# Performance work log

Measured on AMD Instinct MI355X. Metric: run time of the kernel, lower is better.

## Reference

```python
import jax, jax.numpy as jnp
import numpy as np

BETA = 0.25

def setup_inputs() -> dict:
    key = jax.random.key(0)
    k1, k2 = jax.random.split(key)
    x = jax.random.normal(k1, (32, 1024, 256), dtype=jnp.float32)
    # tf.random_uniform_initializer default range is [-0.05, 0.05)
    embedding = jax.random.uniform(k2, (256, 8192), dtype=jnp.float32, minval=-0.05, maxval=0.05)
    return {"x": x, "embedding": embedding}


def reference(x, embedding):
    # x: [B, S, D]; embedding: [D, K] (codebook stored column-wise, as in the tf module)
    D = x.shape[-1]
    flat = x.reshape(-1, D)                                   # [N, D]
    dists = (jnp.sum(flat * flat, axis=1, keepdims=True)
             - 2.0 * (flat @ embedding)
             + jnp.sum(embedding * embedding, axis=0))
    idx = jnp.argmin(dists, axis=1)                           # [N] int
    quantized = jnp.take(embedding.T, idx, axis=0).reshape(x.shape)  # gather codebook columns
    # VQ losses
    commitment = jnp.mean(jnp.square(jax.lax.stop_gradient(quantized) - x))
    codebook = jnp.mean(jnp.square(quantized - jax.lax.stop_gradient(x)))
    loss = BETA * commitment + codebook
    # straight-through estimator
    quantized_st = x + jax.lax.stop_gradient(quantized - x)
    return quantized_st, loss
```

## Files before the change

kernel.cpp:

```cpp
#include <hip/hip_runtime.h>

typedef float f4   __attribute__((ext_vector_type(4)));
typedef float f2   __attribute__((ext_vector_type(2)));
typedef _Float16 f16x8 __attribute__((ext_vector_type(8)));
typedef float f32x4  __attribute__((ext_vector_type(4)));

#define N_ROWS  32768
#define D_DIM   256
#define K_CODES 8192
#define NUM_ELEM (N_ROWS * D_DIM)
#define EPS_MARGIN 2e-3f
#define FB_CAP  8192
#define FB_RPB  16
#define RF_SLICES 32
#define N_PANELS 256
#define HALF_PANELS 128

__device__ __forceinline__ void gl2lds16(const void* g, void* l) {
    __builtin_amdgcn_global_load_lds(
        (const __attribute__((address_space(1))) unsigned int*)g,
        (__attribute__((address_space(3))) unsigned int*)l, 16, 0, 0);
}

__global__ void prep_kernel(const float* __restrict__ E, short* __restrict__ Ep,
                            float* __restrict__ Et32, float* __restrict__ ee,
                            float* __restrict__ ctl) {
    __shared__ float eepart[8][32];
    const int p  = blockIdx.x;
    const int t  = threadIdx.x;
    const int c  = t & 31;
    const int gq = t >> 5;
    const int cp = p * 32;
    if (p == 0) {
        f4 z = (f4)(0.0f);
        f4* dst = (f4*)ctl;
        dst[t * 2]     = z;
        dst[t * 2 + 1] = z;
    }
    short* ph = Ep + (size_t)p * 8192;
    float ss = 0.0f;
    #pragma unroll
    for (int gi = 0; gi < 4; ++gi) {
        int g = gq * 4 + gi;
        f16x8 h;
        f4 av, bv;
        #pragma unroll
        for (int j = 0; j < 8; ++j) {
            float v = E[(size_t)(g * 8 + j) * K_CODES + cp + c];
            h[j] = (_Float16)v;
            ss += v * v;
            if (j < 4) av[j] = v; else bv[j - 4] = v;
        }
        *(f16x8*)(ph + (g * 32 + c) * 8) = h;
        *(f4*)(Et32 + (size_t)(cp + c) * D_DIM + g * 8)     = av;
        *(f4*)(Et32 + (size_t)(cp + c) * D_DIM + g * 8 + 4) = bv;
    }
    eepart[gq][c] = ss;
    __syncthreads();
    if (t < 32) {
        float s = 0.0f;
        #pragma unroll
        for (int q = 0; q < 8; ++q) s += eepart[q][t];
        ee[cp + t] = s;
    }
}

__launch_bounds__(256, 2)
__global__ void mfma_sieve_kernel(const float* __restrict__ X,
                                  const short* __restrict__ Ep,
                                  const float* __restrict__ ee,
                                  f2* __restrict__ res_bs,
                                  int* __restrict__ res_idx) {
    __shared__ __align__(16) short Bbuf[2][8192];
    const int t    = threadIdx.x;
    const int w    = t >> 6;
    const int lane = t & 63;
    const int n    = lane & 15;
    const int quad = lane >> 4;
    const int half = blockIdx.x & 1;
    const int row0 = (blockIdx.x >> 1) * 128;
    const int rw   = row0 + w * 32;
    const int p0   = half * HALF_PANELS;

    f16x8 Ah[2][8];
    #pragma unroll
    for (int rt = 0; rt < 2; ++rt) {
        const float* xp = X + (size_t)(rw + rt * 16 + n) * D_DIM;
        #pragma unroll
        for (int ks = 0; ks < 8; ++ks) {
            int d = ks * 32 + quad * 8;
            f4 a = *(const f4*)(xp + d);
            f4 b = *(const f4*)(xp + d + 4);
            f16x8 h;
            #pragma unroll
            for (int j = 0; j < 8; ++j) {
                float x = (j < 4) ? a[j] : b[j - 4];
                h[j] = (_Float16)x;
            }
            Ah[rt][ks] = h;
        }
    }

    float bestv[8], secv[8]; int besti[8];
    #pragma unroll
    for (int s = 0; s < 8; ++s) { bestv[s] = 1e30f; secv[s] = 1e30f; besti[s] = 0; }

    {
        const char* gp = (const char*)Ep + (size_t)p0 * 16384;
        char* lp = (char*)&Bbuf[0][0];
        #pragma unroll
        for (int i = 0; i < 4; ++i)
            gl2lds16(gp + (w * 4 + i) * 1024 + lane * 16, lp + (w * 4 + i) * 1024);
    }
    __syncthreads();

    for (int i = 0; i < HALF_PANELS; ++i) {
        const int p   = p0 + i;
        const int buf = i & 1;
        if (i + 1 < HALF_PANELS) {
            const char* gp = (const char*)Ep + (size_t)(p + 1) * 16384;
            char* lp = (char*)&Bbuf[buf ^ 1][0];
            #pragma unroll
            for (int k = 0; k < 4; ++k)
                gl2lds16(gp + (w * 4 + k) * 1024 + lane * 16, lp + (w * 4 + k) * 1024);
        }

        const short* Bh = &Bbuf[buf][0];

        f32x4 acc[2][2];
        #pragma unroll
        for (int ct = 0; ct < 2; ++ct)
            #pragma unroll
            for (int rt = 0; rt < 2; ++rt)
                acc[ct][rt] = (f32x4)(0.0f);

        #pragma unroll
        for (int ks = 0; ks < 8; ++ks) {
            const int g = ks * 4 + quad;
            f16x8 bh[2];
            #pragma unroll
            for (int ct = 0; ct < 2; ++ct) {
                int c = ct * 16 + n;
                bh[ct] = *(const f16x8*)(Bh + (g * 32 + c) * 8);
            }
            #pragma unroll
            for (int ct = 0; ct < 2; ++ct)
                #pragma unroll
                for (int rt = 0; rt < 2; ++rt)
                    acc[ct][rt] = __builtin_amdgcn_mfma_f32_16x16x32_f16(Ah[rt][ks], bh[ct], acc[ct][rt], 0, 0, 0);
        }

        const int cb = p * 32;
        #pragma unroll
        for (int ct = 0; ct < 2; ++ct) {
            int code = cb + ct * 16 + n;
            float eev = ee[code];
            #pragma unroll
            for (int rt = 0; rt < 2; ++rt)
                #pragma unroll
                for (int r = 0; r < 4; ++r) {
                    float key = fmaf(-2.0f, acc[ct][rt][r], eev);
                    int s = rt * 4 + r;
                    float nb = fminf(key, bestv[s]);
                    secv[s]  = fminf(secv[s], fmaxf(key, bestv[s]));
                    besti[s] = (key < bestv[s]) ? code : besti[s];
                    bestv[s] = nb;
                }
        }
        __syncthreads();
    }

    #pragma unroll
    for (int off = 1; off < 16; off <<= 1) {
        #pragma unroll
        for (int s = 0; s < 8; ++s) {
            float ov = __shfl_xor(bestv[s], off);
            int   oi = __shfl_xor(besti[s], off);
            float os = __shfl_xor(secv[s], off);
            bool owin = (ov < bestv[s]) || (ov == bestv[s] && oi < besti[s]);
            if (owin) { secv[s] = fminf(os, bestv[s]); bestv[s] = ov; besti[s] = oi; }
            else      { secv[s] = fminf(secv[s], ov); }
        }
    }

    if (n == 0) {
        #pragma unroll
        for (int s = 0; s < 8; ++s) {
            int rl  = w * 32 + (s >> 2) * 16 + quad * 4 + (s & 3);
            int row = row0 + rl;
            f2 bs; bs[0] = bestv[s]; bs[1] = secv[s];
            res_bs[(size_t)row * 2 + half]  = bs;
            res_idx[(size_t)row * 2 + half] = besti[s];
        }
    }
}

__global__ void gather_kernel(const float* __restrict__ X, const float* __restrict__ Et32,
                              const f2* __restrict__ res_bs, const int* __restrict__ res_idx,
                              int* __restrict__ counter, int2* __restrict__ list,
                              float* __restrict__ out, double* __restrict__ loss_sum) {
    __shared__ int bl_[128];
    const int t    = threadIdx.x;
    const int row0 = blockIdx.x * 128;
    if (t < 128) {
        const int row = row0 + t;
        f2 a = res_bs[(size_t)row * 2];
        f2 b = res_bs[(size_t)row * 2 + 1];
        int ia = res_idx[(size_t)row * 2];
        int ib = res_idx[(size_t)row * 2 + 1];
        float gb; int gi; float gs;
        if (b[0] < a[0]) { gb = b[0]; gi = ib; gs = fminf(b[1], a[0]); }
        else             { gb = a[0]; gi = ia; gs = fminf(a[1], b[0]); }
        bl_[t] = gi;
        if (gs - gb <= EPS_MARGIN) {
            int pos = atomicAdd(counter, 1);
            if (pos < FB_CAP) list[pos] = make_int2(row, gi);
        }
    }
    __syncthreads();
    double ls = 0.0;
    const int d = t;
    #pragma unroll 4
    for (int r = 0; r < 128; ++r) {
        int code = bl_[r];
        float q  = Et32[(size_t)code * D_DIM + d];
        float x  = X[(size_t)(row0 + r) * D_DIM + d];
        float dq = q - x;
        out[(size_t)(row0 + r) * D_DIM + d] = x + dq;
        ls += (double)dq * (double)dq;
    }
    #pragma unroll
    for (int off = 32; off > 0; off >>= 1)
        ls += __shfl_down(ls, off);
    if ((t & 63) == 0) atomicAdd(loss_sum, ls);
}

__global__ void refine1_kernel(const float* __restrict__ X, const float* __restrict__ E,
                               const int* __restrict__ counter, const int2* __restrict__ list,
                               double* __restrict__ res_v, int* __restrict__ res_i) {
    __shared__ double xt[FB_RPB][D_DIM];
    __shared__ int rows_sh[FB_RPB];
    __shared__ double wbv[4][FB_RPB];
    __shared__ int    wbi[4][FB_RPB];

    int nf = *counter; if (nf > FB_CAP) nf = FB_CAP;
    const int nchunks = (nf + FB_RPB - 1) / FB_RPB;
    const int nitems  = nchunks * RF_SLICES;
    const int t = threadIdx.x;

    for (int item = blockIdx.x; item < nitems; item += gridDim.x) {
        const int rc = item / RF_SLICES;
        const int sl = item % RF_SLICES;
        __syncthreads();
        if (t < FB_RPB) {
            int e = rc * FB_RPB + t;
            int2 ent = list[(e < nf) ? e : 0];
            rows_sh[t] = ent.x;
        }
        __syncthreads();
        #pragma unroll
        for (int j = 0; j < FB_RPB; ++j)
            xt[j][t] = (double)X[(size_t)rows_sh[j] * D_DIM + t];
        __syncthreads();

        const int k0 = sl * 256 + t;
        double s[FB_RPB], q = 0.0;
        #pragma unroll
        for (int j = 0; j < FB_RPB; ++j) s[j] = 0.0;
        for (int d = 0; d < D_DIM; ++d) {
            double e0d = (double)E[(size_t)d * K_CODES + k0];
            q += e0d * e0d;
            #pragma unroll
            for (int j = 0; j < FB_RPB; ++j)
                s[j] += xt[j][d] * e0d;
        }
        double bv[FB_RPB]; int bi[FB_RPB];
        #pragma unroll
        for (int j = 0; j < FB_RPB; ++j) { bv[j] = q - 2.0 * s[j]; bi[j] = k0; }
        #pragma unroll
        for (int off = 1; off < 64; off <<= 1) {
            #pragma unroll
            for (int j = 0; j < FB_RPB; ++j) {
                double ov = __shfl_xor(bv[j], off);
                int    oi = __shfl_xor(bi[j], off);
                if (ov < bv[j] || (ov == bv[j] && oi < bi[j])) { bv[j] = ov; bi[j] = oi; }
            }
        }
        const int wave = t >> 6;
        if ((t & 63) == 0) {
            #pragma unroll
            for (int j = 0; j < FB_RPB; ++j) { wbv[wave][j] = bv[j]; wbi[wave][j] = bi[j]; }
        }
        __syncthreads();
        if (t < FB_RPB) {
            double b = wbv[0][t]; int i_ = wbi[0][t];
            #pragma unroll
            for (int wv = 1; wv < 4; ++wv) {
                double ov = wbv[wv][t]; int oi = wbi[wv][t];
                if (ov < b || (ov == b && oi < i_)) { b = ov; i_ = oi; }
            }
            int e = rc * FB_RPB + t;
            res_v[(size_t)e * RF_SLICES + sl] = b;
            res_i[(size_t)e * RF_SLICES + sl] = i_;
        }
    }
}

__global__ void patch_kernel(const float* __restrict__ X, const float* __restrict__ Et32,
                             float* __restrict__ out, double* __restrict__ loss_sum,
                             const int* __restrict__ counter, const int2* __restrict__ list,
                             const double* __restrict__ res_v, const int* __restrict__ res_i) {
    int nf = *counter; if (nf > FB_CAP) nf = FB_CAP;
    __shared__ int nc_sh;
    const int t = threadIdx.x;
    for (int b = blockIdx.x; b < nf; b += gridDim.x) {
        __syncthreads();
        if (t == 0) {
            double bv = res_v[(size_t)b * RF_SLICES]; int bi = res_i[(size_t)b * RF_SLICES];
            for (int s = 1; s < RF_SLICES; ++s) {
                double v = res_v[(size_t)b * RF_SLICES + s];
                int    i = res_i[(size_t)b * RF_SLICES + s];
                if (v < bv || (v == bv && i < bi)) { bv = v; bi = i; }
            }
            nc_sh = bi;
        }
        __syncthreads();
        int2 ent = list[b];
        const int oc = ent.y, row = ent.x, nc = nc_sh;
        if (nc != oc) {
            float x  = X[(size_t)row * D_DIM + t];
            float qn = Et32[(size_t)nc * D_DIM + t];
            float qo = Et32[(size_t)oc * D_DIM + t];
            float dqn = qn - x, dqo = qo - x;
            out[(size_t)row * D_DIM + t] = x + dqn;
            double dl = (double)dqn * dqn - (double)dqo * dqo;
            #pragma unroll
            for (int off = 32; off > 0; off >>= 1)
                dl += __shfl_down(dl, off);
            if ((t & 63) == 0) atomicAdd(loss_sum, dl);
        }
    }
}

__global__ void fin_kernel(const double* __restrict__ loss_sum, float* __restrict__ out) {
    double m = loss_sum[0] / (double)NUM_ELEM;
    out[NUM_ELEM] = (float)(0.25 * m + m);
}

extern "C" void kernel_launch(void* const* d_in, const int* in_sizes, int n_in,
                              void* d_out, int out_size, void* d_ws, size_t ws_size,
                              hipStream_t stream) {
    const float* X = (const float*)d_in[0];
    const float* E = (const float*)d_in[1];
    float* out = (float*)d_out;

    double* loss_sum = (double*)d_ws;
    int*    counter  = (int*)((char*)d_ws + 8);
    float*  ee       = (float*)((char*)d_ws + 8192);
    int2*   list     = (int2*)((char*)d_ws + 40960);
    double* res_v    = (double*)((char*)d_ws + 131072);
    int*    res_i    = (int*)((char*)d_ws + 2228224);
    float*  Et32     = (float*)((char*)d_ws + 4194304);
    short*  Ep       = (short*)((char*)d_ws + 12582912);
    f2*     res_bs   = (f2*)((char*)d_ws + 16777216);
    int*    res_idx  = (int*)((char*)d_ws + 17301504);

    prep_kernel<<<N_PANELS, 256, 0, stream>>>(E, Ep, Et32, ee, (float*)d_ws);
    mfma_sieve_kernel<<<512, 256, 0, stream>>>(X, Ep, ee, res_bs, res_idx);
    gather_kernel<<<N_ROWS / 128, 256, 0, stream>>>(X, Et32, res_bs, res_idx,
                                                    counter, list, out, loss_sum);
    refine1_kernel<<<1024, 256, 0, stream>>>(X, E, counter, list, res_v, res_i);
    patch_kernel<<<1024, 256, 0, stream>>>(X, Et32, out, loss_sum, counter, list,
                                           res_v, res_i);
    fin_kernel<<<1, 1, 0, stream>>>(loss_sum, out);
}
```

Measured before the change: 329.5 us.

## Fuse gather into sieve via last-arriver counter and fold finalize into patch

The separate gather kernel is removed. Each 128-row tile's two half-codebook sieve blocks bump a per-tile ready counter, and the second block to arrive merges both halves and writes the output rows and loss. The finalize kernel is likewise folded into the patch kernel, where the last block to finish computes the loss. This removes two kernel launches and lets gather work overlap with sieve blocks still running. In exchange it adds atomics and fences, and relies on the ready and patch_done counters being zeroed in workspace every call.

New measurement: 503.7 us. 52.9% more time.

```diff
diff --git a/kernel.cpp b/kernel.cpp
--- a/kernel.cpp
+++ b/kernel.cpp
@@ -69,16 +69,23 @@
 __global__ void mfma_sieve_kernel(const float* __restrict__ X,
                                   const short* __restrict__ Ep,
                                   const float* __restrict__ ee,
+                                  const float* __restrict__ Et32,
                                   f2* __restrict__ res_bs,
-                                  int* __restrict__ res_idx) {
+                                  int* __restrict__ res_idx,
+                                  int* __restrict__ ready,
+                                  int* __restrict__ counter, int2* __restrict__ list,
+                                  float* __restrict__ out, double* __restrict__ loss_sum) {
     __shared__ __align__(16) short Bbuf[2][8192];
+    __shared__ int bl2_[128];
+    __shared__ int do_gather;
     const int t    = threadIdx.x;
     const int w    = t >> 6;
     const int lane = t & 63;
     const int n    = lane & 15;
     const int quad = lane >> 4;
     const int half = blockIdx.x & 1;
-    const int row0 = (blockIdx.x >> 1) * 128;
+    const int rtile = blockIdx.x >> 1;
+    const int row0 = rtile * 128;
     const int rw   = row0 + w * 32;
     const int p0   = half * HALF_PANELS;
 
@@ -193,25 +200,29 @@
             res_idx[(size_t)row * 2 + half] = besti[s];
         }
     }
-}
-
-__global__ void gather_kernel(const float* __restrict__ X, const float* __restrict__ Et32,
-                              const f2* __restrict__ res_bs, const int* __restrict__ res_idx,
-                              int* __restrict__ counter, int2* __restrict__ list,
-                              float* __restrict__ out, double* __restrict__ loss_sum) {
-    __shared__ int bl_[128];
-    const int t    = threadIdx.x;
-    const int row0 = blockIdx.x * 128;
+
+    __threadfence();
+    __syncthreads();
+    if (t == 0) {
+        int old = atomicAdd(&ready[rtile], 1);
+        do_gather = (old == 1);
+    }
+    __syncthreads();
+    if (!do_gather) return;
+    __threadfence();
+
     if (t < 128) {
         const int row = row0 + t;
-        f2 a = res_bs[(size_t)row * 2];
-        f2 b = res_bs[(size_t)row * 2 + 1];
-        int ia = res_idx[(size_t)row * 2];
-        int ib = res_idx[(size_t)row * 2 + 1];
+        union { double d; f2 f; } ua, ub;
+        ua.d = atomicAdd((double*)&res_bs[(size_t)row * 2], 0.0);
+        ub.d = atomicAdd((double*)&res_bs[(size_t)row * 2 + 1], 0.0);
+        int ia = atomicOr(&res_idx[(size_t)row * 2], 0);
+        int ib = atomicOr(&res_idx[(size_t)row * 2 + 1], 0);
+        f2 a = ua.f, b = ub.f;
         float gb; int gi; float gs;
         if (b[0] < a[0]) { gb = b[0]; gi = ib; gs = fminf(b[1], a[0]); }
         else             { gb = a[0]; gi = ia; gs = fminf(a[1], b[0]); }
-        bl_[t] = gi;
+        bl2_[t] = gi;
         if (gs - gb <= EPS_MARGIN) {
             int pos = atomicAdd(counter, 1);
             if (pos < FB_CAP) list[pos] = make_int2(row, gi);
@@ -222,7 +233,7 @@
     const int d = t;
     #pragma unroll 4
     for (int r = 0; r < 128; ++r) {
-        int code = bl_[r];
+        int code = bl2_[r];
         float q  = Et32[(size_t)code * D_DIM + d];
         float x  = X[(size_t)(row0 + r) * D_DIM + d];
         float dq = q - x;
@@ -309,7 +320,8 @@
 __global__ void patch_kernel(const float* __restrict__ X, const float* __restrict__ Et32,
                              float* __restrict__ out, double* __restrict__ loss_sum,
                              const int* __restrict__ counter, const int2* __restrict__ list,
-                             const double* __restrict__ res_v, const int* __restrict__ res_i) {
+                             const double* __restrict__ res_v, const int* __restrict__ res_i,
+                             int* __restrict__ patch_done) {
     int nf = *counter; if (nf > FB_CAP) nf = FB_CAP;
     __shared__ int nc_sh;
     const int t = threadIdx.x;
@@ -340,11 +352,15 @@
             if ((t & 63) == 0) atomicAdd(loss_sum, dl);
         }
     }
-}
-
-__global__ void fin_kernel(const double* __restrict__ loss_sum, float* __restrict__ out) {
-    double m = loss_sum[0] / (double)NUM_ELEM;
-    out[NUM_ELEM] = (float)(0.25 * m + m);
+    __threadfence();
+    __syncthreads();
+    if (t == 0) {
+        int old = atomicAdd(patch_done, 1);
+        if (old == (int)gridDim.x - 1) {
+            double m = atomicAdd(loss_sum, 0.0) / (double)NUM_ELEM;
+            out[NUM_ELEM] = (float)(0.25 * m + m);
+        }
+    }
 }
 
 extern "C" void kernel_launch(void* const* d_in, const int* in_sizes, int n_in,
@@ -354,23 +370,23 @@
     const float* E = (const float*)d_in[1];
     float* out = (float*)d_out;
 
-    double* loss_sum = (double*)d_ws;
-    int*    counter  = (int*)((char*)d_ws + 8);
-    float*  ee       = (float*)((char*)d_ws + 8192);
-    int2*   list     = (int2*)((char*)d_ws + 40960);
-    double* res_v    = (double*)((char*)d_ws + 131072);
-    int*    res_i    = (int*)((char*)d_ws + 2228224);
-    float*  Et32     = (float*)((char*)d_ws + 4194304);
-    short*  Ep       = (short*)((char*)d_ws + 12582912);
-    f2*     res_bs   = (f2*)((char*)d_ws + 16777216);
-    int*    res_idx  = (int*)((char*)d_ws + 17301504);
+    double* loss_sum   = (double*)d_ws;
+    int*    counter    = (int*)((char*)d_ws + 8);
+    int*    patch_done = (int*)((char*)d_ws + 16);
+    int*    ready      = (int*)((char*)d_ws + 1024);
+    float*  ee         = (float*)((char*)d_ws + 8192);
+    int2*   list       = (int2*)((char*)d_ws + 40960);
+    double* res_v      = (double*)((char*)d_ws + 131072);
+    int*    res_i      = (int*)((char*)d_ws + 2228224);
+    float*  Et32       = (float*)((char*)d_ws + 4194304);
+    short*  Ep         = (short*)((char*)d_ws + 12582912);
+    f2*     res_bs     = (f2*)((char*)d_ws + 16777216);
+    int*    res_idx    = (int*)((char*)d_ws + 17301504);
 
     prep_kernel<<<N_PANELS, 256, 0, stream>>>(E, Ep, Et32, ee, (float*)d_ws);
-    mfma_sieve_kernel<<<512, 256, 0, stream>>>(X, Ep, ee, res_bs, res_idx);
-    gather_kernel<<<N_ROWS / 128, 256, 0, stream>>>(X, Et32, res_bs, res_idx,
-                                                    counter, list, out, loss_sum);
+    mfma_sieve_kernel<<<512, 256, 0, stream>>>(X, Ep, ee, Et32, res_bs, res_idx,
+                                               ready, counter, list, out, loss_sum);
     refine1_kernel<<<1024, 256, 0, stream>>>(X, E, counter, list, res_v, res_i);
     patch_kernel<<<1024, 256, 0, stream>>>(X, Et32, out, loss_sum, counter, list,
-                                           res_v, res_i);
-    fin_kernel<<<1, 1, 0, stream>>>(loss_sum, out);
-}
+                                           res_v, res_i, patch_done);
+}
```
